# Performance work log

Hardware: AMD Instinct MI355X
Metric: run time of the kernel (lower is better)

Reference implementation:

```python
import jax, jax.numpy as jnp
import numpy as np

FORGET_BIAS = 1.0  # tf.nn.rnn_cell.LSTMCell default

def lstm_scan(x_seq, W, b, reverse=False):
    # x_seq: [B, T, D]; W: [D+U, 4U] with TF gate order (i, j, f, o); b: [4U]
    B = x_seq.shape[0]
    U = b.shape[0] // 4
    xs = jnp.swapaxes(x_seq, 0, 1)  # [T, B, D]

    def step(carry, x_t):
        c, h = carry
        z = jnp.dot(jnp.concatenate([x_t, h], axis=-1), W) + b  # [B, 4U]
        i, j, f, o = jnp.split(z, 4, axis=-1)
        c_new = jax.nn.sigmoid(f + FORGET_BIAS) * c + jax.nn.sigmoid(i) * jnp.tanh(j)
        h_new = jax.nn.sigmoid(o) * jnp.tanh(c_new)
        return (c_new, h_new), h_new

    init = (jnp.zeros((B, U), x_seq.dtype), jnp.zeros((B, U), x_seq.dtype))
    _, hs = jax.lax.scan(step, init, xs, reverse=reverse)  # outputs aligned to time index
    return jnp.swapaxes(hs, 0, 1)  # [B, T, U]

def setup_inputs() -> dict:
    key = jax.random.key(0)
    k1, k2, k3 = jax.random.split(key, 3)
    B, H, W_, C = 64, 8, 512, 64
    D, U = H * C, 256
    scale = 1.0 / np.sqrt(D + U)
    x = jax.random.normal(k1, (B, H, W_, C), dtype=jnp.float32)
    W_fw = jax.random.normal(k2, (D + U, 4 * U), dtype=jnp.float32) * scale
    W_bw = jax.random.normal(k3, (D + U, 4 * U), dtype=jnp.float32) * scale
    b_fw = jnp.zeros((4 * U,), dtype=jnp.float32)
    b_bw = jnp.zeros((4 * U,), dtype=jnp.float32)
    return {"x": x, "W_fw": W_fw, "b_fw": b_fw, "W_bw": W_bw, "b_bw": b_bw}

def reference(x, W_fw, b_fw, W_bw, b_bw):
    b, h, w, c = x.shape
    # dropout is identity at inference (training=False)
    feats = jnp.transpose(x, (0, 2, 1, 3)).reshape(b, w, h * c)  # [B, T, D]
    out_fw = lstm_scan(feats, W_fw, b_fw, reverse=False)
    out_bw = lstm_scan(feats, W_bw, b_bw, reverse=True)
    return jnp.concatenate([out_fw, out_bw], axis=2)  # [B, T, 2U]
```

## Files before the change

### kernel.cpp

```cpp
#include <hip/hip_runtime.h>


typedef float f32x4 __attribute__((ext_vector_type(4)));
typedef _Float16 f16;
typedef _Float16 f16x4 __attribute__((ext_vector_type(4)));
typedef _Float16 f16x8 __attribute__((ext_vector_type(8)));
typedef unsigned long long u64;

__global__ void init_all(const float* __restrict__ Wfw, const float* __restrict__ Wbw,
                         f16* __restrict__ wrec2, unsigned int* __restrict__ hbuf_u32,
                         unsigned int* __restrict__ ctr) {
    const int i = blockIdx.x * blockDim.x + threadIdx.x;
    const int dir = i >> 18;
    const int rem = i & 0x3FFFF;
    const int col = rem >> 8;
    const int k   = rem & 255;
    const int sl  = col >> 7;
    const int gg  = (col & 127) >> 5;
    const int uu  = col & 31;
    const float* W = dir ? Wbw : Wfw;
    wrec2[i] = (f16)W[(size_t)(512 + k) * 1024 + gg * 256 + sl * 32 + uu];
    if (i < 32768) hbuf_u32[i] = 0u;
    if (i < 128) ctr[i] = 0u;
}

#define BM 128
#define BN 128
#define BK 32
#define ASTR 40

__global__ __launch_bounds__(256)
void gemm_xz(const float* __restrict__ x,
             const float* __restrict__ Wfw, const float* __restrict__ Wbw,
             const float* __restrict__ bfw, const float* __restrict__ bbw,
             f16* __restrict__ xz_fw, f16* __restrict__ xz_bw) {
    const int dir = blockIdx.z;
    const float* __restrict__ W    = dir ? Wbw : Wfw;
    const float* __restrict__ bias = dir ? bbw : bfw;
    f16* __restrict__ xz = dir ? xz_bw : xz_fw;

    __shared__ __align__(16) f16 As[BM * ASTR];
    __shared__ __align__(16) f16 Bs[BN * ASTR];

    const int tid = threadIdx.x;
    const int m0 = blockIdx.x * BM;
    const int n0 = blockIdx.y * BN;

    const int lane = tid & 63;
    const int wave = tid >> 6;
    const int wm = (wave & 1) * 64;
    const int wn = (wave >> 1) * 64;
    const int mi = lane & 15;
    const int kq = lane >> 4;

    const int arow = tid >> 1;
    const int ahalf = (tid & 1) * 16;
    const int am = m0 + arow;
    const int bb = am >> 9;
    const int t  = am & 511;
    const int kk = tid >> 3;
    const int nc = (tid & 7) * 16;

    f32x4 acc[4][4];
#pragma unroll
    for (int i = 0; i < 4; i++)
#pragma unroll
        for (int j = 0; j < 4; j++) acc[i][j] = (f32x4)0.f;

    for (int kt = 0; kt < 512; kt += BK) {
        float va[16], vb[16];
        {
            const int kbase = kt + ahalf;
            const int hh = kbase >> 6;
            const float* px = x + (((size_t)bb * 8 + hh) * 512 + t) * 64 + (kbase & 63);
#pragma unroll
            for (int i = 0; i < 4; i++) {
                f32x4 v = *(const f32x4*)(px + i * 4);
                va[i*4+0] = v[0]; va[i*4+1] = v[1]; va[i*4+2] = v[2]; va[i*4+3] = v[3];
            }
            const float* pw = W + (size_t)(kt + kk) * 1024 + n0 + nc;
#pragma unroll
            for (int i = 0; i < 4; i++) {
                f32x4 v = *(const f32x4*)(pw + i * 4);
                vb[i*4+0] = v[0]; vb[i*4+1] = v[1]; vb[i*4+2] = v[2]; vb[i*4+3] = v[3];
            }
        }
        __syncthreads();
        {
            f16* pa = &As[arow * ASTR + ahalf];
#pragma unroll
            for (int i = 0; i < 4; i++) {
                f16x4 s;
                s[0] = (f16)va[i*4+0]; s[1] = (f16)va[i*4+1];
                s[2] = (f16)va[i*4+2]; s[3] = (f16)va[i*4+3];
                *(f16x4*)(pa + i * 4) = s;
            }
#pragma unroll
            for (int i = 0; i < 16; i++)
                Bs[(nc + i) * ASTR + kk] = (f16)vb[i];
        }
        __syncthreads();
        f16x8 afr[4], bfr[4];
#pragma unroll
        for (int mt = 0; mt < 4; mt++)
            afr[mt] = *(const f16x8*)(&As[(wm + mt * 16 + mi) * ASTR + kq * 8]);
#pragma unroll
        for (int nt = 0; nt < 4; nt++)
            bfr[nt] = *(const f16x8*)(&Bs[(wn + nt * 16 + mi) * ASTR + kq * 8]);
#pragma unroll
        for (int mt = 0; mt < 4; mt++)
#pragma unroll
            for (int nt = 0; nt < 4; nt++)
                acc[mt][nt] = __builtin_amdgcn_mfma_f32_16x16x32_f16(
                    afr[mt], bfr[nt], acc[mt][nt], 0, 0, 0);
    }

    const int col = lane & 15;
    const int rbase = kq * 4;
#pragma unroll
    for (int mt = 0; mt < 4; mt++) {
#pragma unroll
        for (int nt = 0; nt < 4; nt++) {
            const int n = n0 + wn + nt * 16 + col;
            const float bv = bias[n];
#pragma unroll
            for (int r = 0; r < 4; r++) {
                const int mrow = m0 + wm + mt * 16 + rbase + r;
                xz[(size_t)mrow * 1024 + n] = (f16)(acc[mt][nt][r] + bv);
            }
        }
    }
}

#define AP 264
#define ZP 67

__global__ __launch_bounds__(256, 1)
void rec_persist(const f16* __restrict__ xz, const f16* __restrict__ wrec2,
                 f16* __restrict__ hbuf, unsigned int* __restrict__ ctr,
                 float* __restrict__ out) {
    const int bid = blockIdx.x;
    const int dir = bid >> 3;
    const int sl  = bid & 7;
    const f16* __restrict__ xzd = xz + (size_t)dir * 64 * 512 * 1024;
    const f16* __restrict__ wsl = wrec2 + ((size_t)dir * 1024 + sl * 128) * 256;
    f16* __restrict__ hbd = hbuf + (size_t)dir * 2 * 64 * 256;
    unsigned int* __restrict__ myc = ctr + dir * 64;

    __shared__ __align__(16) f16  A_lds[64 * AP];
    __shared__ float z_lds[128 * ZP];

    const int tid = threadIdx.x;
    const int lane = tid & 63;
    const int w = tid >> 6;
    const int r = w >> 1, c = w & 1;
    const int mi = lane & 15, kq = lane >> 4;

    f16x8 Bf[4][8];
#pragma unroll
    for (int nt = 0; nt < 4; nt++)
#pragma unroll
        for (int ks = 0; ks < 8; ks++)
            Bf[nt][ks] = *(const f16x8*)(wsl + (size_t)(c * 64 + nt * 16 + mi) * 256
                                             + ks * 32 + kq * 8);

    const int b_act = tid >> 2;
    const int ug = tid & 3;
    float cell[8];
#pragma unroll
    for (int j = 0; j < 8; j++) cell[j] = 0.f;

    const int sm = tid >> 2;

    float pv[8];
    int   pt = 0;

    float* const outb = out + ((size_t)b_act * 512) * 512 + dir * 256 + sl * 32 + ug * 8;

    for (int s = 0; s < 512; s++) {
        const int t = dir ? (511 - s) : s;

        u64 va[16];
        {
            const u64* src = (const u64*)(hbd + (s & 1) * (64 * 256) + sm * 256);
#pragma unroll
            for (int i = 0; i < 16; i++)
                va[i] = __hip_atomic_load(src + i * 4 + ug, __ATOMIC_RELAXED,
                                          __HIP_MEMORY_SCOPE_AGENT);
        }
        if (s) {
            float* op = outb + (size_t)pt * 512;
            f32x4 o0 = {pv[0], pv[1], pv[2], pv[3]};
            f32x4 o1 = {pv[4], pv[5], pv[6], pv[7]};
            *(f32x4*)op = o0;
            *(f32x4*)(op + 4) = o1;
        }
        f16x8 xzv[4];
        const f16* xp = xzd + ((size_t)b_act * 512 + t) * 1024 + sl * 32 + ug * 8;
#pragma unroll
        for (int g = 0; g < 4; g++) xzv[g] = *(const f16x8*)(xp + g * 256);

        {
            f16* dst = A_lds + sm * AP;
#pragma unroll
            for (int i = 0; i < 16; i++)
                *(u64*)(dst + i * 16 + ug * 4) = va[i];
        }
        __syncthreads();

        f32x4 acc[2][4];
#pragma unroll
        for (int mt = 0; mt < 2; mt++)
#pragma unroll
            for (int nt = 0; nt < 4; nt++) acc[mt][nt] = (f32x4)0.f;
#pragma unroll
        for (int ks = 0; ks < 8; ks++) {
            f16x8 Af[2];
#pragma unroll
            for (int mt = 0; mt < 2; mt++)
                Af[mt] = *(const f16x8*)(A_lds + (r * 32 + mt * 16 + mi) * AP
                                               + ks * 32 + kq * 8);
#pragma unroll
            for (int mt = 0; mt < 2; mt++)
#pragma unroll
                for (int nt = 0; nt < 4; nt++)
                    acc[mt][nt] = __builtin_amdgcn_mfma_f32_16x16x32_f16(
                        Af[mt], Bf[nt][ks], acc[mt][nt], 0, 0, 0);
        }
#pragma unroll
        for (int mt = 0; mt < 2; mt++)
#pragma unroll
            for (int nt = 0; nt < 4; nt++) {
                const int col = c * 64 + nt * 16 + mi;
                float* zp = z_lds + col * ZP + r * 32 + mt * 16 + kq * 4;
#pragma unroll
                for (int ri = 0; ri < 4; ri++) zp[ri] = acc[mt][nt][ri];
            }
        __syncthreads();

        float hv[8];
#pragma unroll
        for (int j = 0; j < 8; j++) {
            const int uu = ug * 8 + j;
            const float zi = z_lds[(0 * 32 + uu) * ZP + b_act] + (float)xzv[0][j];
            const float zj = z_lds[(1 * 32 + uu) * ZP + b_act] + (float)xzv[1][j];
            const float zf = z_lds[(2 * 32 + uu) * ZP + b_act] + (float)xzv[2][j] + 1.0f;
            const float zo = z_lds[(3 * 32 + uu) * ZP + b_act] + (float)xzv[3][j];
            const float si = 1.f / (1.f + __expf(-zi));
            const float sf = 1.f / (1.f + __expf(-zf));
            const float so = 1.f / (1.f + __expf(-zo));
            const float tj = 1.f - 2.f / (1.f + __expf(2.f * zj));
            cell[j] = sf * cell[j] + si * tj;
            hv[j] = so * (1.f - 2.f / (1.f + __expf(2.f * cell[j])));
        }
        union { f16 h[8]; u64 q[2]; } up;
#pragma unroll
        for (int j = 0; j < 8; j++) up.h[j] = (f16)hv[j];
        f16* hwp = hbd + ((s + 1) & 1) * (64 * 256) + b_act * 256 + sl * 32 + ug * 8;
        __hip_atomic_store((u64*)hwp, up.q[0], __ATOMIC_RELAXED, __HIP_MEMORY_SCOPE_AGENT);
        __hip_atomic_store((u64*)hwp + 1, up.q[1], __ATOMIC_RELAXED, __HIP_MEMORY_SCOPE_AGENT);
#pragma unroll
        for (int j = 0; j < 8; j++) pv[j] = hv[j];
        pt = t;

        __syncthreads();
        if (tid == 0)
            __hip_atomic_fetch_add(myc, 1u, __ATOMIC_RELAXED, __HIP_MEMORY_SCOPE_AGENT);
        const unsigned tgt = 8u * (unsigned)(s + 1);
        while (__hip_atomic_load(myc, __ATOMIC_RELAXED, __HIP_MEMORY_SCOPE_AGENT) < tgt)
            __builtin_amdgcn_s_sleep(1);
    }
    {
        float* op = outb + (size_t)pt * 512;
        f32x4 o0 = {pv[0], pv[1], pv[2], pv[3]};
        f32x4 o1 = {pv[4], pv[5], pv[6], pv[7]};
        *(f32x4*)op = o0;
        *(f32x4*)(op + 4) = o1;
    }
}

extern "C" void kernel_launch(void* const* d_in, const int* in_sizes, int n_in,
                              void* d_out, int out_size, void* d_ws, size_t ws_size,
                              hipStream_t stream) {
    const float* x   = (const float*)d_in[0];
    const float* Wfw = (const float*)d_in[1];
    const float* bfw = (const float*)d_in[2];
    const float* Wbw = (const float*)d_in[3];
    const float* bbw = (const float*)d_in[4];
    float* out = (float*)d_out;

    f16* xzf   = (f16*)d_ws;
    f16* xzb   = xzf + (size_t)64 * 512 * 1024;
    f16* wrec2 = xzb + (size_t)64 * 512 * 1024;
    f16* hbuf  = wrec2 + (size_t)2 * 1024 * 256;
    unsigned int* ctr = (unsigned int*)(hbuf + (size_t)2 * 2 * 64 * 256);

    init_all<<<dim3(2048), 256, 0, stream>>>(Wfw, Wbw, wrec2, (unsigned int*)hbuf, ctr);
    gemm_xz<<<dim3(256, 8, 2), 256, 0, stream>>>(x, Wfw, Wbw, bfw, bbw, xzf, xzb);
    rec_persist<<<dim3(16), 256, 0, stream>>>(xzf, wrec2, hbuf, ctr, out);

    (void)in_sizes; (void)n_in; (void)out_size; (void)ws_size;
}
```

Measured before the change: 2.753 ms.

## Replace global counter barrier with step-tagged hidden-state words for dataflow sync

Each fp16 hidden value is now stored in a 32-bit word alongside a 16-bit step tag. Readers spin on their own loads until every tag matches the current step, which removes the per-step __syncthreads plus the atomic-counter barrier across the 8 blocks of each direction. The cost is twice the traffic on the hidden buffer, unpacking work before the LDS store, and a MAXSPIN bailout that could silently use stale data if a producer is delayed too long.

```diff
diff --git a/kernel.cpp b/kernel.cpp
--- a/kernel.cpp
+++ b/kernel.cpp
@@ -5,11 +5,11 @@
 typedef _Float16 f16;
 typedef _Float16 f16x4 __attribute__((ext_vector_type(4)));
 typedef _Float16 f16x8 __attribute__((ext_vector_type(8)));
+typedef unsigned int u32;
 typedef unsigned long long u64;
 
 __global__ void init_all(const float* __restrict__ Wfw, const float* __restrict__ Wbw,
-                         f16* __restrict__ wrec2, unsigned int* __restrict__ hbuf_u32,
-                         unsigned int* __restrict__ ctr) {
+                         f16* __restrict__ wrec2, u32* __restrict__ hbuf) {
     const int i = blockIdx.x * blockDim.x + threadIdx.x;
     const int dir = i >> 18;
     const int rem = i & 0x3FFFF;
@@ -20,8 +20,7 @@
     const int uu  = col & 31;
     const float* W = dir ? Wbw : Wfw;
     wrec2[i] = (f16)W[(size_t)(512 + k) * 1024 + gg * 256 + sl * 32 + uu];
-    if (i < 32768) hbuf_u32[i] = 0u;
-    if (i < 128) ctr[i] = 0u;
+    if (i < 65536) hbuf[i] = 0u;
 }
 
 #define BM 128
@@ -134,18 +133,17 @@
 
 #define AP 264
 #define ZP 67
+#define MAXSPIN 20000
 
 __global__ __launch_bounds__(256, 1)
 void rec_persist(const f16* __restrict__ xz, const f16* __restrict__ wrec2,
-                 f16* __restrict__ hbuf, unsigned int* __restrict__ ctr,
-                 float* __restrict__ out) {
+                 u32* __restrict__ hbuf, float* __restrict__ out) {
     const int bid = blockIdx.x;
     const int dir = bid >> 3;
     const int sl  = bid & 7;
     const f16* __restrict__ xzd = xz + (size_t)dir * 64 * 512 * 1024;
     const f16* __restrict__ wsl = wrec2 + ((size_t)dir * 1024 + sl * 128) * 256;
-    f16* __restrict__ hbd = hbuf + (size_t)dir * 2 * 64 * 256;
-    unsigned int* __restrict__ myc = ctr + dir * 64;
+    u32* __restrict__ hbd = hbuf + (size_t)dir * 2 * 64 * 256;
 
     __shared__ __align__(16) f16  A_lds[64 * AP];
     __shared__ float z_lds[128 * ZP];
@@ -180,14 +178,18 @@
     for (int s = 0; s < 512; s++) {
         const int t = dir ? (511 - s) : s;
 
-        u64 va[16];
-        {
-            const u64* src = (const u64*)(hbd + (s & 1) * (64 * 256) + sm * 256);
-#pragma unroll
-            for (int i = 0; i < 16; i++)
-                va[i] = __hip_atomic_load(src + i * 4 + ug, __ATOMIC_RELAXED,
+        const u64* src = (const u64*)(hbd + (s & 1) * (64 * 256)) + (size_t)sm * 128;
+        const u64 tpat = ((u64)(u32)s << 16) | ((u64)(u32)s << 48);
+
+        u64 va[32];
+#pragma unroll
+        for (int i = 0; i < 16; i++) {
+            va[2*i]   = __hip_atomic_load(src + i * 8 + ug * 2,     __ATOMIC_RELAXED,
                                           __HIP_MEMORY_SCOPE_AGENT);
-        }
+            va[2*i+1] = __hip_atomic_load(src + i * 8 + ug * 2 + 1, __ATOMIC_RELAXED,
+                                          __HIP_MEMORY_SCOPE_AGENT);
+        }
+
         if (s) {
             float* op = outb + (size_t)pt * 512;
             f32x4 o0 = {pv[0], pv[1], pv[2], pv[3]};
@@ -200,11 +202,32 @@
 #pragma unroll
         for (int g = 0; g < 4; g++) xzv[g] = *(const f16x8*)(xp + g * 256);
 
+        int spins = 0;
+        for (;;) {
+            u64 bad = 0;
+#pragma unroll
+            for (int i = 0; i < 32; i++)
+                bad |= (va[i] ^ tpat) & 0xFFFF0000FFFF0000ull;
+            if (!__any(bad != 0)) break;
+            if (++spins > MAXSPIN) break;
+            if (spins > 8) __builtin_amdgcn_s_sleep(1);
+#pragma unroll
+            for (int i = 0; i < 16; i++) {
+                va[2*i]   = __hip_atomic_load(src + i * 8 + ug * 2,     __ATOMIC_RELAXED,
+                                              __HIP_MEMORY_SCOPE_AGENT);
+                va[2*i+1] = __hip_atomic_load(src + i * 8 + ug * 2 + 1, __ATOMIC_RELAXED,
+                                              __HIP_MEMORY_SCOPE_AGENT);
+            }
+        }
+
         {
             f16* dst = A_lds + sm * AP;
 #pragma unroll
-            for (int i = 0; i < 16; i++)
-                *(u64*)(dst + i * 16 + ug * 4) = va[i];
+            for (int i = 0; i < 16; i++) {
+                u32 p0 = (u32)(va[2*i]   & 0xFFFFull) | ((u32)(va[2*i]   >> 32) << 16);
+                u32 p1 = (u32)(va[2*i+1] & 0xFFFFull) | ((u32)(va[2*i+1] >> 32) << 16);
+                *(u64*)(dst + i * 16 + ug * 4) = (u64)p0 | ((u64)p1 << 32);
+            }
         }
         __syncthreads();
 
@@ -253,22 +276,23 @@
             cell[j] = sf * cell[j] + si * tj;
             hv[j] = so * (1.f - 2.f / (1.f + __expf(2.f * cell[j])));
         }
-        union { f16 h[8]; u64 q[2]; } up;
-#pragma unroll
-        for (int j = 0; j < 8; j++) up.h[j] = (f16)hv[j];
-        f16* hwp = hbd + ((s + 1) & 1) * (64 * 256) + b_act * 256 + sl * 32 + ug * 8;
-        __hip_atomic_store((u64*)hwp, up.q[0], __ATOMIC_RELAXED, __HIP_MEMORY_SCOPE_AGENT);
-        __hip_atomic_store((u64*)hwp + 1, up.q[1], __ATOMIC_RELAXED, __HIP_MEMORY_SCOPE_AGENT);
+        {
+            const u32 tg1 = (u32)(s + 1);
+            u32* hwp = hbd + ((s + 1) & 1) * (64 * 256) + b_act * 256 + sl * 32 + ug * 8;
+            union { f16 h; unsigned short us; } cv;
+#pragma unroll
+            for (int p = 0; p < 4; p++) {
+                cv.h = (f16)hv[2*p];
+                u64 q = (u64)cv.us | ((u64)tg1 << 16);
+                cv.h = (f16)hv[2*p+1];
+                q |= ((u64)cv.us << 32) | ((u64)tg1 << 48);
+                __hip_atomic_store((u64*)hwp + p, q, __ATOMIC_RELAXED,
+                                   __HIP_MEMORY_SCOPE_AGENT);
+            }
+        }
 #pragma unroll
         for (int j = 0; j < 8; j++) pv[j] = hv[j];
         pt = t;
-
-        __syncthreads();
-        if (tid == 0)
-            __hip_atomic_fetch_add(myc, 1u, __ATOMIC_RELAXED, __HIP_MEMORY_SCOPE_AGENT);
-        const unsigned tgt = 8u * (unsigned)(s + 1);
-        while (__hip_atomic_load(myc, __ATOMIC_RELAXED, __HIP_MEMORY_SCOPE_AGENT) < tgt)
-            __builtin_amdgcn_s_sleep(1);
     }
     {
         float* op = outb + (size_t)pt * 512;
@@ -292,12 +316,11 @@
     f16* xzf   = (f16*)d_ws;
     f16* xzb   = xzf + (size_t)64 * 512 * 1024;
     f16* wrec2 = xzb + (size_t)64 * 512 * 1024;
-    f16* hbuf  = wrec2 + (size_t)2 * 1024 * 256;
-    unsigned int* ctr = (unsigned int*)(hbuf + (size_t)2 * 2 * 64 * 256);
-
-    init_all<<<dim3(2048), 256, 0, stream>>>(Wfw, Wbw, wrec2, (unsigned int*)hbuf, ctr);
+    u32* hbuf  = (u32*)(wrec2 + (size_t)2 * 1024 * 256);
+
+    init_all<<<dim3(2048), 256, 0, stream>>>(Wfw, Wbw, wrec2, hbuf);
     gemm_xz<<<dim3(256, 8, 2), 256, 0, stream>>>(x, Wfw, Wbw, bfw, bbw, xzf, xzb);
-    rec_persist<<<dim3(16), 256, 0, stream>>>(xzf, wrec2, hbuf, ctr, out);
+    rec_persist<<<dim3(16), 256, 0, stream>>>(xzf, wrec2, hbuf, out);
 
     (void)in_sizes; (void)n_in; (void)out_size; (void)ws_size;
 }
```

Measured after the change: 3.579 ms. +30.0%, slower.
